# Optimization experiments

Hardware: AMD Instinct MI355X
Metric: run time of the kernel (lower is better)

## Reference

```python
import jax, jax.numpy as jnp
import numpy as np

N = 20000
E = 320000
IN_DIM = 16
H = 128
HEADS = 4
NEG_SLOPE = 0.2  # GATv2Conv default
EPS_LN = 1e-5


def setup_inputs() -> dict:
    key = jax.random.key(0)
    ks = jax.random.split(key, 16)
    f32 = jnp.float32
    def rn(k, shape, scale):
        return jax.random.normal(k, shape, dtype=f32) * scale
    s_in = 1.0 / np.sqrt(IN_DIM)
    s_h = 1.0 / np.sqrt(H)
    s_4h = 1.0 / np.sqrt(4 * H)
    s_2h = 1.0 / np.sqrt(2 * H)
    inp = {}
    inp["x"] = jax.random.normal(ks[0], (N, IN_DIM), dtype=f32)
    inp["edge_index"] = jax.random.randint(ks[1], (2, E), 0, N)
    inp["edge_attr"] = jax.random.normal(ks[2], (E, 2), dtype=f32)
    inp["emb_w"] = rn(ks[3], (IN_DIM, H), s_in)
    inp["emb_b"] = jnp.zeros((H,), f32)
    # 3 GATv2 layers stacked on leading axis
    inp["lin_l"] = rn(ks[4], (3, H, HEADS * H), s_h)
    inp["lin_r"] = rn(ks[5], (3, H, HEADS * H), s_h)
    inp["lin_edge"] = rn(ks[6], (3, 2, HEADS * H), 1.0 / np.sqrt(2.0))
    inp["att"] = rn(ks[7], (3, HEADS, H), s_h)
    inp["conv_bias01"] = jnp.zeros((2, HEADS * H), f32)  # concat=True layers
    inp["conv_bias2"] = jnp.zeros((H,), f32)             # concat=False layer
    inp["proj_w"] = rn(ks[8], (2, HEADS * H, H), s_4h)
    inp["proj_b"] = jnp.zeros((2, H), f32)
    inp["n1_g"] = jnp.ones((3, H), f32)
    inp["n1_b"] = jnp.zeros((3, H), f32)
    inp["n2_g"] = jnp.ones((3, H), f32)
    inp["n2_b"] = jnp.zeros((3, H), f32)
    inp["ffn_w1"] = rn(ks[9], (3, H, 2 * H), s_h)
    inp["ffn_b1"] = jnp.zeros((3, 2 * H), f32)
    inp["ffn_w2"] = rn(ks[10], (3, 2 * H, H), s_2h)
    inp["ffn_b2"] = jnp.zeros((3, H), f32)
    return inp


def layer_norm(x, g, b):
    mu = jnp.mean(x, axis=-1, keepdims=True)
    var = jnp.mean((x - mu) ** 2, axis=-1, keepdims=True)
    return (x - mu) * jax.lax.rsqrt(var + EPS_LN) * g + b


def gatv2(h, src, dst, eattr, Wl, Wr, We, att, bias, concat, n):
    # h: [n, H]; per-edge gather -> GATv2 attention -> segment softmax -> scatter-add
    xl = (h @ Wl).reshape(n, HEADS, H)   # source transform
    xr = (h @ Wr).reshape(n, HEADS, H)   # target transform
    ee = (eattr @ We).reshape(-1, HEADS, H)
    e = jax.nn.leaky_relu(xl[src] + xr[dst] + ee, NEG_SLOPE)  # [E', HEADS, H]
    score = jnp.einsum('ehc,hc->eh', e, att)                  # [E', HEADS]
    smax = jax.ops.segment_max(score, dst, num_segments=n)
    p = jnp.exp(score - smax[dst])
    denom = jax.ops.segment_sum(p, dst, num_segments=n)
    alpha = p / (denom[dst] + 1e-16)
    out = jax.ops.segment_sum(xl[src] * alpha[..., None], dst, num_segments=n)
    if concat:
        return out.reshape(n, HEADS * H) + bias
    return jnp.mean(out, axis=1) + bias


def reference(x, edge_index, edge_attr, emb_w, emb_b, lin_l, lin_r, lin_edge, att,
              conv_bias01, conv_bias2, proj_w, proj_b, n1_g, n1_b, n2_g, n2_b,
              ffn_w1, ffn_b1, ffn_w2, ffn_b2):
    n = x.shape[0]
    e = edge_attr.shape[0]
    # PyG add_self_loops with fill_value='mean': self-loop attr = mean of incoming edge attrs
    ones = jnp.ones((e,), x.dtype)
    deg = jax.ops.segment_sum(ones, edge_index[1], num_segments=n)
    loop_attr = jax.ops.segment_sum(edge_attr, edge_index[1], num_segments=n) / jnp.maximum(deg, 1.0)[:, None]
    ar = jnp.arange(n)
    src = jnp.concatenate([edge_index[0], ar])
    dst = jnp.concatenate([edge_index[1], ar])
    ea = jnp.concatenate([edge_attr, loop_attr], axis=0)

    h = x @ emb_w + emb_b
    for i in range(3):
        concat = i < 2
        bias = conv_bias01[i] if concat else conv_bias2
        h_in = h
        h = gatv2(h, src, dst, ea, lin_l[i], lin_r[i], lin_edge[i], att[i], bias, concat, n)
        if concat:
            h = h @ proj_w[i] + proj_b[i]
        h = layer_norm(h + h_in, n1_g[i], n1_b[i])
        h2 = h
        h = jax.nn.gelu(h @ ffn_w1[i] + ffn_b1[i], approximate=False) @ ffn_w2[i] + ffn_b2[i]
        h = layer_norm(h + h2, n2_g[i], n2_b[i])
    return h
```

## Files before the change

kernel.cpp:

```cpp
#include <hip/hip_runtime.h>
#include <math.h>

#define IN_DIM 16
#define HDIM   128
#define HEADS  4
#define HH     512
#define FFH    256
#define NEG_SLOPE 0.2f

typedef _Float16 half8 __attribute__((ext_vector_type(8)));
typedef _Float16 h8 __attribute__((ext_vector_type(8)));
typedef _Float16 h4 __attribute__((ext_vector_type(4)));
typedef _Float16 h2 __attribute__((ext_vector_type(2)));
typedef float f32x4 __attribute__((ext_vector_type(4)));

struct __align__(8) Edge { int src; _Float16 ea0, ea1; };

static __device__ inline float hsum8(h8 v) {
    h4 a = __builtin_shufflevector(v, v, 0, 1, 2, 3) +
           __builtin_shufflevector(v, v, 4, 5, 6, 7);
    h2 b = __builtin_shufflevector(a, a, 0, 1) +
           __builtin_shufflevector(a, a, 2, 3);
    return (float)b[0] + (float)b[1];
}

__global__ void xpad_kernel(const float* __restrict__ x, _Float16* __restrict__ xh, int n) {
    int idx = blockIdx.x * 256 + threadIdx.x;
    if (idx >= n * 64) return;
    int r = idx >> 6, k = idx & 63;
    xh[idx] = (k < IN_DIM) ? (_Float16)x[r * IN_DIM + k] : (_Float16)0.0f;
}

struct WDesc { const float* src; _Float16* dst; int Ksrc; int lgKd; int lgN; };
struct WDescs { WDesc d[15]; };
__global__ void wconv_kernel(WDescs ds) {
    WDesc w = ds.d[blockIdx.y];
    int Kd = 1 << w.lgKd;
    int total = 1 << (w.lgKd + w.lgN);
    for (int idx = blockIdx.x * 256 + threadIdx.x; idx < total; idx += gridDim.x * 256) {
        int n2 = idx >> w.lgKd, k = idx & (Kd - 1);
        w.dst[idx] = (k < w.Ksrc) ? (_Float16)w.src[(k << w.lgN) + n2] : (_Float16)0.0f;
    }
}

__global__ void deg_kernel(const int* __restrict__ ei, const float* __restrict__ eattr,
                           float* deg, float* asum, int E) {
    int e = blockIdx.x * blockDim.x + threadIdx.x;
    if (e >= E) return;
    int d = ei[E + e];
    atomicAdd(&deg[d], 1.0f);
    atomicAdd(&asum[2 * d], eattr[2 * e]);
    atomicAdd(&asum[2 * d + 1], eattr[2 * e + 1]);
}

__global__ void scan_kernel(const float* __restrict__ deg, int* row_ptr, int* cur, int n) {
    __shared__ int sums[1024];
    int tid = threadIdx.x;
    int per = (n + 1023) / 1024;
    int s0 = tid * per;
    int s1 = s0 + per; if (s1 > n) s1 = n;
    int s = 0;
    for (int i = s0; i < s1; i++) s += (int)deg[i] + 1;
    int mysum = s;
    sums[tid] = s;
    __syncthreads();
    for (int dd = 1; dd < 1024; dd <<= 1) {
        int t = (tid >= dd) ? sums[tid - dd] : 0;
        __syncthreads();
        sums[tid] += t;
        __syncthreads();
    }
    int run = sums[tid] - mysum;
    for (int i = s0; i < s1; i++) {
        row_ptr[i] = run; cur[i] = run;
        run += (int)deg[i] + 1;
    }
    if (tid == 1023) row_ptr[n] = sums[1023];
}

__global__ void scatter_kernel(const int* __restrict__ ei, const float* __restrict__ eattr,
                               const float* __restrict__ deg, const float* __restrict__ asum,
                               int* cur, Edge* csr, int E, int n) {
    int i = blockIdx.x * blockDim.x + threadIdx.x;
    if (i >= E + n) return;
    Edge ed;
    int pos;
    if (i < E) {
        int d = ei[E + i];
        pos = atomicAdd(&cur[d], 1);
        ed.src = ei[i];
        ed.ea0 = (_Float16)eattr[2 * i];
        ed.ea1 = (_Float16)eattr[2 * i + 1];
    } else {
        int nd = i - E;
        float dv = fmaxf(deg[nd], 1.0f);
        pos = atomicAdd(&cur[nd], 1);
        ed.src = nd;
        ed.ea0 = (_Float16)(asum[2 * nd] / dv);
        ed.ea1 = (_Float16)(asum[2 * nd + 1] / dv);
    }
    csr[pos] = ed;
}

template <int ACT, int OUTMODE, int BM>
__global__ __launch_bounds__(256) void gemm_mfma(const _Float16* __restrict__ A, int lda,
                                                 const _Float16* __restrict__ BT,
                                                 const float* __restrict__ bias,
                                                 float* __restrict__ C32,
                                                 _Float16* __restrict__ C16,
                                                 int M, int N, int K) {
    const int BK = 64, PAD = 8, NI = BM / 32;
    __shared__ _Float16 As[BM][BK + PAD];
    __shared__ _Float16 Bs[128][BK + PAD];
    int tid = threadIdx.x;
    int wave = tid >> 6, lane = tid & 63;
    int quad = lane >> 4, l16 = lane & 15;
    int wrow = (wave >> 1) * (16 * NI);
    int wcol = (wave & 1) * 64;
    int mBase = blockIdx.y * BM;
    int n0 = blockIdx.x * 128;

    f32x4 acc[NI][4] = {};

    for (int k0 = 0; k0 < K; k0 += BK) {
#pragma unroll
        for (int t = 0; t < BM / 32; t++) {
            int idx = tid + t * 256;
            int r = idx >> 3, kb = (idx & 7) * 8;
            half8 hv = {};
            int grow = mBase + r;
            if (grow < M) hv = *(const half8*)(A + (size_t)grow * lda + k0 + kb);
            *(half8*)&As[r][kb] = hv;
        }
#pragma unroll
        for (int t = 0; t < 4; t++) {
            int idx = tid + t * 256;
            int r = idx >> 3, kb = (idx & 7) * 8;
            *(half8*)&Bs[r][kb] = *(const half8*)(BT + (size_t)(n0 + r) * K + k0 + kb);
        }
        __syncthreads();
#pragma unroll
        for (int kc = 0; kc < 2; kc++) {
            half8 a[NI], b[4];
#pragma unroll
            for (int i = 0; i < NI; i++)
                a[i] = *(const half8*)&As[wrow + i * 16 + l16][kc * 32 + quad * 8];
#pragma unroll
            for (int j = 0; j < 4; j++)
                b[j] = *(const half8*)&Bs[wcol + j * 16 + l16][kc * 32 + quad * 8];
#pragma unroll
            for (int i = 0; i < NI; i++)
#pragma unroll
                for (int j = 0; j < 4; j++)
                    acc[i][j] = __builtin_amdgcn_mfma_f32_16x16x32_f16(a[i], b[j], acc[i][j], 0, 0, 0);
        }
        __syncthreads();
    }

#pragma unroll
    for (int i = 0; i < NI; i++) {
#pragma unroll
        for (int r = 0; r < 4; r++) {
            int row = mBase + wrow + i * 16 + quad * 4 + r;
            if (row >= M) continue;
#pragma unroll
            for (int j = 0; j < 4; j++) {
                int col = n0 + wcol + j * 16 + l16;
                float v = acc[i][j][r] + (bias ? bias[col] : 0.0f);
                if (ACT == 1) v = 0.5f * v * (1.0f + erff(v * 0.70710678118654752f));
                if (OUTMODE == 0 || OUTMODE == 2)
                    C32[(size_t)row * N + col] = v;
                if (OUTMODE == 1 || OUTMODE == 2)
                    C16[(size_t)row * N + col] = (_Float16)v;
            }
        }
    }
}

__global__ __launch_bounds__(256) void gemm_ln(const _Float16* __restrict__ A, int lda,
                                               const _Float16* __restrict__ BT,
                                               const float* __restrict__ bias,
                                               const float* __restrict__ R,
                                               const float* __restrict__ g,
                                               const float* __restrict__ b,
                                               float* __restrict__ C32,
                                               _Float16* __restrict__ C16,
                                               int M, int K) {
    const int BK = 64, PAD = 8;
    __shared__ _Float16 As[64][BK + PAD];
    __shared__ _Float16 Bs[128][BK + PAD];
    int tid = threadIdx.x;
    int wave = tid >> 6, lane = tid & 63;
    int quad = lane >> 4, l16 = lane & 15;
    int mBase = blockIdx.x * 64;

    f32x4 acc[8] = {};

    for (int k0 = 0; k0 < K; k0 += BK) {
#pragma unroll
        for (int t = 0; t < 2; t++) {
            int idx = tid + t * 256;
            int r = idx >> 3, kb = (idx & 7) * 8;
            half8 hv = {};
            int grow = mBase + r;
            if (grow < M) hv = *(const half8*)(A + (size_t)grow * lda + k0 + kb);
            *(half8*)&As[r][kb] = hv;
        }
#pragma unroll
        for (int t = 0; t < 4; t++) {
            int idx = tid + t * 256;
            int r = idx >> 3, kb = (idx & 7) * 8;
            *(half8*)&Bs[r][kb] = *(const half8*)(BT + (size_t)r * K + k0 + kb);
        }
        __syncthreads();
#pragma unroll
        for (int kc = 0; kc < 2; kc++) {
            half8 a = *(const half8*)&As[wave * 16 + l16][kc * 32 + quad * 8];
#pragma unroll
            for (int j = 0; j < 8; j++) {
                half8 bb = *(const half8*)&Bs[j * 16 + l16][kc * 32 + quad * 8];
                acc[j] = __builtin_amdgcn_mfma_f32_16x16x32_f16(a, bb, acc[j], 0, 0, 0);
            }
        }
        __syncthreads();
    }

    float gj[8], bj[8], biasj[8];
#pragma unroll
    for (int j = 0; j < 8; j++) {
        int col = j * 16 + l16;
        biasj[j] = bias[col];
        gj[j] = g[col];
        bj[j] = b[col];
    }
    int row0 = mBase + wave * 16 + quad * 4;
    float sum[4] = {}, sq[4] = {};
#pragma unroll
    for (int r = 0; r < 4; r++) {
        int row = row0 + r;
        bool ok = row < M;
        size_t base = (size_t)row * HDIM;
#pragma unroll
        for (int j = 0; j < 8; j++) {
            float v = acc[j][r] + biasj[j] + (ok ? R[base + j * 16 + l16] : 0.0f);
            acc[j][r] = v;
            sum[r] += v;
            sq[r] += v * v;
        }
    }
#pragma unroll
    for (int r = 0; r < 4; r++) {
#pragma unroll
        for (int off = 1; off < 16; off <<= 1) {
            sum[r] += __shfl_xor(sum[r], off);
            sq[r] += __shfl_xor(sq[r], off);
        }
    }
#pragma unroll
    for (int r = 0; r < 4; r++) {
        int row = row0 + r;
        if (row >= M) continue;
        size_t base = (size_t)row * HDIM;
        float mu = sum[r] * (1.0f / HDIM);
        float var = sq[r] * (1.0f / HDIM) - mu * mu;
        float invstd = rsqrtf(var + 1e-5f);
#pragma unroll
        for (int j = 0; j < 8; j++) {
            float o = (acc[j][r] - mu) * invstd * gj[j] + bj[j];
            C32[base + j * 16 + l16] = o;
            if (C16) C16[base + j * 16 + l16] = (_Float16)o;
        }
    }
}

__global__ __launch_bounds__(256) void gat_edge_kernel(
    const _Float16* __restrict__ XLR,
    const int* __restrict__ row_ptr, const Edge* __restrict__ csr,
    const float* __restrict__ We,
    const float* __restrict__ attW,
    const float* __restrict__ cbias,
    _Float16* __restrict__ OUT16, float* __restrict__ OUT32, int n, int concat) {
    int tid = threadIdx.x;
    int wave = tid >> 6, lane = tid & 63;
    int node = blockIdx.x * 4 + wave;
    if (node >= n) return;
    int c0 = lane * 8;

    h8 xr8 = *(const h8*)(XLR + (size_t)node * 1024 + 512 + c0);
    h8 w08, w18, att8;
#pragma unroll
    for (int k = 0; k < 8; k++) {
        w08[k] = (_Float16)We[c0 + k];
        w18[k] = (_Float16)We[HH + c0 + k];
        att8[k] = (_Float16)attW[c0 + k];
    }
    const _Float16 slope = (_Float16)NEG_SLOPE;

    h8 acc2 = (h8)(_Float16)0.0f;
    float m = -INFINITY, l = 0.0f;
    int beg = row_ptr[node], end = row_ptr[node + 1];
    int j = beg;
    for (; j + 1 < end; j += 2) {
        Edge e0 = csr[j], e1 = csr[j + 1];
        h8 x0 = *(const h8*)(XLR + (size_t)e0.src * 1024 + c0);
        h8 x1 = *(const h8*)(XLR + (size_t)e1.src * 1024 + c0);
        h8 v0 = x0 + (xr8 + w08 * e0.ea0 + w18 * e0.ea1);
        h8 v1 = x1 + (xr8 + w08 * e1.ea0 + w18 * e1.ea1);
        v0 = __builtin_elementwise_max(v0, v0 * slope);
        v1 = __builtin_elementwise_max(v1, v1 * slope);
        float p0 = hsum8(v0 * att8);
        float p1 = hsum8(v1 * att8);
        p0 += __shfl_xor(p0, 1); p1 += __shfl_xor(p1, 1);
        p0 += __shfl_xor(p0, 2); p1 += __shfl_xor(p1, 2);
        p0 += __shfl_xor(p0, 4); p1 += __shfl_xor(p1, 4);
        p0 += __shfl_xor(p0, 8); p1 += __shfl_xor(p1, 8);
        float mnew = fmaxf(m, fmaxf(p0, p1));
        float sc = __expf(m - mnew);
        float e0f = __expf(p0 - mnew);
        float e1f = __expf(p1 - mnew);
        l = l * sc + e0f + e1f;
        acc2 = acc2 * (_Float16)sc + x0 * (_Float16)e0f + x1 * (_Float16)e1f;
        m = mnew;
    }
    if (j < end) {
        Edge e0 = csr[j];
        h8 x0 = *(const h8*)(XLR + (size_t)e0.src * 1024 + c0);
        h8 v0 = x0 + (xr8 + w08 * e0.ea0 + w18 * e0.ea1);
        v0 = __builtin_elementwise_max(v0, v0 * slope);
        float p0 = hsum8(v0 * att8);
        p0 += __shfl_xor(p0, 1);
        p0 += __shfl_xor(p0, 2);
        p0 += __shfl_xor(p0, 4);
        p0 += __shfl_xor(p0, 8);
        float mnew = fmaxf(m, p0);
        float sc = __expf(m - mnew);
        float e0f = __expf(p0 - mnew);
        l = l * sc + e0f;
        acc2 = acc2 * (_Float16)sc + x0 * (_Float16)e0f;
        m = mnew;
    }
    float invf = 1.0f / (l + 1e-16f);
    if (concat) {
        h8 o = acc2 * (_Float16)invf;
#pragma unroll
        for (int k = 0; k < 8; k++) o[k] = o[k] + (_Float16)cbias[c0 + k];
        *(h8*)(OUT16 + (size_t)node * 1024 + c0) = o;
    } else {
        float o8[8];
#pragma unroll
        for (int k = 0; k < 8; k++) {
            float a = (float)acc2[k] * invf;
            a += __shfl_xor(a, 16);
            a += __shfl_xor(a, 32);
            o8[k] = a;
        }
        if (lane < 16) {
#pragma unroll
            for (int k = 0; k < 8; k++)
                OUT32[(size_t)node * HDIM + c0 + k] = o8[k] * 0.25f + cbias[c0 + k];
        }
    }
}

__global__ __launch_bounds__(256) void ln_res_kernel(const float* X, const float* R,
                                                     const float* __restrict__ g,
                                                     const float* __restrict__ b,
                                                     float* OUT32, _Float16* OUT16, int n) {
    int wave = threadIdx.x >> 6, lane = threadIdx.x & 63;
    int row = blockIdx.x * 4 + wave;
    if (row >= n) return;
    int c = lane * 2;
    size_t base = (size_t)row * HDIM;
    float x0 = X[base + c] + R[base + c];
    float x1 = X[base + c + 1] + R[base + c + 1];
    float s = x0 + x1;
#pragma unroll
    for (int off = 1; off < 64; off <<= 1) s += __shfl_xor(s, off);
    float mu = s * (1.0f / HDIM);
    float d0 = x0 - mu, d1 = x1 - mu;
    float vs = d0 * d0 + d1 * d1;
#pragma unroll
    for (int off = 1; off < 64; off <<= 1) vs += __shfl_xor(vs, off);
    float invstd = rsqrtf(vs * (1.0f / HDIM) + 1e-5f);
    float o0 = d0 * invstd * g[c] + b[c];
    float o1 = d1 * invstd * g[c + 1] + b[c + 1];
    OUT32[base + c] = o0;
    OUT32[base + c + 1] = o1;
    if (OUT16) {
        OUT16[base + c] = (_Float16)o0;
        OUT16[base + c + 1] = (_Float16)o1;
    }
}

extern "C" void kernel_launch(void* const* d_in, const int* in_sizes, int n_in,
                              void* d_out, int out_size, void* d_ws, size_t ws_size,
                              hipStream_t stream) {
    const float* x        = (const float*)d_in[0];
    const int*   ei       = (const int*)d_in[1];
    const float* eattr    = (const float*)d_in[2];
    const float* emb_w    = (const float*)d_in[3];
    const float* emb_b    = (const float*)d_in[4];
    const float* lin_l    = (const float*)d_in[5];
    const float* lin_r    = (const float*)d_in[6];
    const float* lin_edge = (const float*)d_in[7];
    const float* attw     = (const float*)d_in[8];
    const float* cb01     = (const float*)d_in[9];
    const float* cb2      = (const float*)d_in[10];
    const float* proj_w   = (const float*)d_in[11];
    const float* proj_b   = (const float*)d_in[12];
    const float* n1g      = (const float*)d_in[13];
    const float* n1b      = (const float*)d_in[14];
    const float* n2g      = (const float*)d_in[15];
    const float* n2b      = (const float*)d_in[16];
    const float* fw1      = (const float*)d_in[17];
    const float* fb1      = (const float*)d_in[18];
    const float* fw2      = (const float*)d_in[19];
    const float* fb2      = (const float*)d_in[20];
    float* out = (float*)d_out;

    const int n = in_sizes[0] / IN_DIM;
    const int E = in_sizes[2] / 2;
    const int EP = E + n;

    size_t off = 0;
    auto alloc = [&](size_t bytes) {
        void* p = (char*)d_ws + off;
        off += (bytes + 255) & ~(size_t)255;
        return p;
    };
    float* deg     = (float*)alloc((size_t)n * 4);
    float* asum    = (float*)alloc((size_t)2 * n * 4);
    int*   row_ptr = (int*)alloc((size_t)(n + 1) * 4);
    int*   cur     = (int*)alloc((size_t)n * 4);
    Edge*  csr     = (Edge*)alloc((size_t)EP * 8);
    float* H0      = (float*)alloc((size_t)n * HDIM * 4);
    float* H1      = (float*)alloc((size_t)n * HDIM * 4);
    _Float16* H0h  = (_Float16*)alloc((size_t)n * HDIM * 2);
    _Float16* H1h  = (_Float16*)alloc((size_t)n * HDIM * 2);
    _Float16* MID  = (_Float16*)alloc((size_t)n * FFH * 2);
    _Float16* XLR  = (_Float16*)alloc((size_t)n * 1024 * 2);
    _Float16* xh   = (_Float16*)alloc((size_t)n * 64 * 2);
    _Float16* wt_emb  = (_Float16*)alloc((size_t)HDIM * 64 * 2);
    _Float16* wt_llr  = (_Float16*)alloc((size_t)3 * 1024 * HDIM * 2);
    _Float16* wt_proj = (_Float16*)alloc((size_t)2 * HDIM * HH * 2);
    _Float16* wt_f1   = (_Float16*)alloc((size_t)3 * FFH * HDIM * 2);
    _Float16* wt_f2   = (_Float16*)alloc((size_t)3 * HDIM * FFH * 2);
    (void)ws_size;

    xpad_kernel<<<(n * 64 + 255) / 256, 256, 0, stream>>>(x, xh, n);
    WDescs ds;
    int di = 0;
    ds.d[di++] = {emb_w, wt_emb, IN_DIM, 6, 7};
    for (int i = 0; i < 3; i++) {
        ds.d[di++] = {lin_l + (size_t)i * HDIM * HH, wt_llr + (size_t)i * 1024 * HDIM, HDIM, 7, 9};
        ds.d[di++] = {lin_r + (size_t)i * HDIM * HH, wt_llr + (size_t)i * 1024 * HDIM + (size_t)512 * HDIM, HDIM, 7, 9};
    }
    for (int i = 0; i < 2; i++)
        ds.d[di++] = {proj_w + (size_t)i * HH * HDIM, wt_proj + (size_t)i * HDIM * HH, HH, 9, 7};
    for (int i = 0; i < 3; i++)
        ds.d[di++] = {fw1 + (size_t)i * HDIM * FFH, wt_f1 + (size_t)i * FFH * HDIM, HDIM, 7, 8};
    for (int i = 0; i < 3; i++)
        ds.d[di++] = {fw2 + (size_t)i * FFH * HDIM, wt_f2 + (size_t)i * HDIM * FFH, FFH, 8, 7};
    wconv_kernel<<<dim3(32, 15), 256, 0, stream>>>(ds);

    (void)hipMemsetAsync(deg, 0, (size_t)n * 4, stream);
    (void)hipMemsetAsync(asum, 0, (size_t)2 * n * 4, stream);
    deg_kernel<<<(E + 255) / 256, 256, 0, stream>>>(ei, eattr, deg, asum, E);
    scan_kernel<<<1, 1024, 0, stream>>>(deg, row_ptr, cur, n);
    scatter_kernel<<<(EP + 255) / 256, 256, 0, stream>>>(ei, eattr, deg, asum, cur, csr, E, n);

    gemm_mfma<0, 2, 128><<<dim3(1, (n + 127) / 128), 256, 0, stream>>>(
        xh, 64, wt_emb, emb_b, H0, H0h, n, HDIM, 64);

    for (int i = 0; i < 3; i++) {
        int concat = (i < 2);
        gemm_mfma<0, 1, 128><<<dim3(8, (n + 127) / 128), 256, 0, stream>>>(
            H0h, HDIM, wt_llr + (size_t)i * 1024 * HDIM, nullptr, nullptr, XLR, n, 1024, HDIM);
        gat_edge_kernel<<<(n + 3) / 4, 256, 0, stream>>>(
            XLR, row_ptr, csr,
            lin_edge + (size_t)i * 2 * HH, attw + (size_t)i * HH,
            concat ? (cb01 + (size_t)i * HH) : cb2,
            XLR + 512, H1, n, concat);
        if (concat) {
            gemm_ln<<<(n + 63) / 64, 256, 0, stream>>>(
                XLR + 512, 1024, wt_proj + (size_t)i * HDIM * HH,
                proj_b + (size_t)i * HDIM, H0,
                n1g + (size_t)i * HDIM, n1b + (size_t)i * HDIM,
                H1, H1h, n, HH);
        } else {
            ln_res_kernel<<<(n + 3) / 4, 256, 0, stream>>>(
                H1, H0, n1g + (size_t)i * HDIM, n1b + (size_t)i * HDIM, H1, H1h, n);
        }
        gemm_mfma<1, 1, 128><<<dim3(2, (n + 127) / 128), 256, 0, stream>>>(
            H1h, HDIM, wt_f1 + (size_t)i * FFH * HDIM, fb1 + (size_t)i * FFH,
            nullptr, MID, n, FFH, HDIM);
        float* lnout = (i == 2) ? out : H0;
        _Float16* lnout16 = (i == 2) ? nullptr : H0h;
        gemm_ln<<<(n + 63) / 64, 256, 0, stream>>>(
            MID, FFH, wt_f2 + (size_t)i * HDIM * FFH, fb2 + (size_t)i * HDIM, H1,
            n2g + (size_t)i * HDIM, n2b + (size_t)i * HDIM,
            lnout, lnout16, n, FFH);
    }
}
```

Before: 659.6 us.

## Fuse FFN GEMMs with GELU in shared memory and fold final LayerNorm into GAT kernel

Adds an ffn_fused kernel that computes the first FFN GEMM with bias and GELU, keeps the 64x256 intermediate in shared memory, then runs the second GEMM with bias, residual and LayerNorm. This removes the global MID buffer round trip and one launch per layer. The non-concat GAT layer now applies its residual LayerNorm directly in the edge kernel, so the separate ln_res_kernel launch goes away. The costs are reloading weight tiles per 64-row block, more shared memory per block (lower occupancy), and a serialized GEMM chain inside one block.

```diff
diff --git a/kernel.cpp b/kernel.cpp
--- a/kernel.cpp
+++ b/kernel.cpp
@@ -102,7 +102,7 @@
     csr[pos] = ed;
 }
 
-template <int ACT, int OUTMODE, int BM>
+template <int OUTMODE, int BM>
 __global__ __launch_bounds__(256) void gemm_mfma(const _Float16* __restrict__ A, int lda,
                                                  const _Float16* __restrict__ BT,
                                                  const float* __restrict__ bias,
@@ -167,7 +167,6 @@
             for (int j = 0; j < 4; j++) {
                 int col = n0 + wcol + j * 16 + l16;
                 float v = acc[i][j][r] + (bias ? bias[col] : 0.0f);
-                if (ACT == 1) v = 0.5f * v * (1.0f + erff(v * 0.70710678118654752f));
                 if (OUTMODE == 0 || OUTMODE == 2)
                     C32[(size_t)row * N + col] = v;
                 if (OUTMODE == 1 || OUTMODE == 2)
@@ -273,13 +272,148 @@
     }
 }
 
+__global__ __launch_bounds__(256) void ffn_fused(const _Float16* __restrict__ A,
+                                                 const _Float16* __restrict__ W1T,
+                                                 const float* __restrict__ b1,
+                                                 const _Float16* __restrict__ W2T,
+                                                 const float* __restrict__ b2,
+                                                 const float* __restrict__ R,
+                                                 const float* __restrict__ g,
+                                                 const float* __restrict__ b,
+                                                 float* __restrict__ C32,
+                                                 _Float16* __restrict__ C16,
+                                                 int M) {
+    __shared__ _Float16 Ws[128][128 + 8];
+    __shared__ _Float16 Mid[64][256 + 8];
+    int tid = threadIdx.x;
+    int wave = tid >> 6, lane = tid & 63;
+    int quad = lane >> 4, l16 = lane & 15;
+    int mBase = blockIdx.x * 64;
+
+    half8 afrag[4];
+    {
+        int row = mBase + wave * 16 + l16;
+#pragma unroll
+        for (int kc = 0; kc < 4; kc++) {
+            if (row < M)
+                afrag[kc] = *(const half8*)(A + (size_t)row * HDIM + kc * 32 + quad * 8);
+            else
+                afrag[kc] = (half8)(_Float16)0.0f;
+        }
+    }
+
+#pragma unroll
+    for (int h = 0; h < 2; h++) {
+        if (h) __syncthreads();
+#pragma unroll
+        for (int t = 0; t < 8; t++) {
+            int idx = tid + t * 256;
+            int r = idx >> 4, kb = (idx & 15) * 8;
+            *(half8*)&Ws[r][kb] = *(const half8*)(W1T + (size_t)(h * 128 + r) * HDIM + kb);
+        }
+        __syncthreads();
+        f32x4 acc[8] = {};
+#pragma unroll
+        for (int kc = 0; kc < 4; kc++) {
+#pragma unroll
+            for (int j = 0; j < 8; j++) {
+                half8 bb = *(const half8*)&Ws[j * 16 + l16][kc * 32 + quad * 8];
+                acc[j] = __builtin_amdgcn_mfma_f32_16x16x32_f16(afrag[kc], bb, acc[j], 0, 0, 0);
+            }
+        }
+#pragma unroll
+        for (int j = 0; j < 8; j++) {
+            float bj1 = b1[h * 128 + j * 16 + l16];
+#pragma unroll
+            for (int r = 0; r < 4; r++) {
+                float v = acc[j][r] + bj1;
+                v = 0.5f * v * (1.0f + erff(v * 0.70710678118654752f));
+                Mid[wave * 16 + quad * 4 + r][h * 128 + j * 16 + l16] = (_Float16)v;
+            }
+        }
+    }
+    __syncthreads();
+
+    f32x4 acc2[8] = {};
+#pragma unroll
+    for (int kc2 = 0; kc2 < 2; kc2++) {
+        if (kc2) __syncthreads();
+#pragma unroll
+        for (int t = 0; t < 8; t++) {
+            int idx = tid + t * 256;
+            int r = idx >> 4, kb = (idx & 15) * 8;
+            *(half8*)&Ws[r][kb] = *(const half8*)(W2T + (size_t)r * FFH + kc2 * 128 + kb);
+        }
+        __syncthreads();
+#pragma unroll
+        for (int kc = 0; kc < 4; kc++) {
+            half8 am = *(const half8*)&Mid[wave * 16 + l16][kc2 * 128 + kc * 32 + quad * 8];
+#pragma unroll
+            for (int j = 0; j < 8; j++) {
+                half8 bb = *(const half8*)&Ws[j * 16 + l16][kc * 32 + quad * 8];
+                acc2[j] = __builtin_amdgcn_mfma_f32_16x16x32_f16(am, bb, acc2[j], 0, 0, 0);
+            }
+        }
+    }
+
+    float gj[8], bj[8], b2j[8];
+#pragma unroll
+    for (int j = 0; j < 8; j++) {
+        int col = j * 16 + l16;
+        b2j[j] = b2[col];
+        gj[j] = g[col];
+        bj[j] = b[col];
+    }
+    int row0 = mBase + wave * 16 + quad * 4;
+    float sum[4] = {}, sq[4] = {};
+#pragma unroll
+    for (int r = 0; r < 4; r++) {
+        int row = row0 + r;
+        bool ok = row < M;
+        size_t base = (size_t)row * HDIM;
+#pragma unroll
+        for (int j = 0; j < 8; j++) {
+            float v = acc2[j][r] + b2j[j] + (ok ? R[base + j * 16 + l16] : 0.0f);
+            acc2[j][r] = v;
+            sum[r] += v;
+            sq[r] += v * v;
+        }
+    }
+#pragma unroll
+    for (int r = 0; r < 4; r++) {
+#pragma unroll
+        for (int off = 1; off < 16; off <<= 1) {
+            sum[r] += __shfl_xor(sum[r], off);
+            sq[r] += __shfl_xor(sq[r], off);
+        }
+    }
+#pragma unroll
+    for (int r = 0; r < 4; r++) {
+        int row = row0 + r;
+        if (row >= M) continue;
+        size_t base = (size_t)row * HDIM;
+        float mu = sum[r] * (1.0f / HDIM);
+        float var = sq[r] * (1.0f / HDIM) - mu * mu;
+        float invstd = rsqrtf(var + 1e-5f);
+#pragma unroll
+        for (int j = 0; j < 8; j++) {
+            float o = (acc2[j][r] - mu) * invstd * gj[j] + bj[j];
+            C32[base + j * 16 + l16] = o;
+            if (C16) C16[base + j * 16 + l16] = (_Float16)o;
+        }
+    }
+}
+
 __global__ __launch_bounds__(256) void gat_edge_kernel(
     const _Float16* __restrict__ XLR,
     const int* __restrict__ row_ptr, const Edge* __restrict__ csr,
     const float* __restrict__ We,
     const float* __restrict__ attW,
     const float* __restrict__ cbias,
-    _Float16* __restrict__ OUT16, float* __restrict__ OUT32, int n, int concat) {
+    _Float16* __restrict__ OUT16, float* __restrict__ OUT32,
+    const float* __restrict__ R, const float* __restrict__ lng,
+    const float* __restrict__ lnb, _Float16* __restrict__ OUT16h,
+    int n, int concat) {
     int tid = threadIdx.x;
     int wave = tid >> 6, lane = tid & 63;
     int node = blockIdx.x * 4 + wave;
@@ -354,41 +488,33 @@
             a += __shfl_xor(a, 32);
             o8[k] = a;
         }
+        float v8[8];
+        float sum = 0.0f, sq = 0.0f;
         if (lane < 16) {
 #pragma unroll
-            for (int k = 0; k < 8; k++)
-                OUT32[(size_t)node * HDIM + c0 + k] = o8[k] * 0.25f + cbias[c0 + k];
-        }
-    }
-}
-
-__global__ __launch_bounds__(256) void ln_res_kernel(const float* X, const float* R,
-                                                     const float* __restrict__ g,
-                                                     const float* __restrict__ b,
-                                                     float* OUT32, _Float16* OUT16, int n) {
-    int wave = threadIdx.x >> 6, lane = threadIdx.x & 63;
-    int row = blockIdx.x * 4 + wave;
-    if (row >= n) return;
-    int c = lane * 2;
-    size_t base = (size_t)row * HDIM;
-    float x0 = X[base + c] + R[base + c];
-    float x1 = X[base + c + 1] + R[base + c + 1];
-    float s = x0 + x1;
-#pragma unroll
-    for (int off = 1; off < 64; off <<= 1) s += __shfl_xor(s, off);
-    float mu = s * (1.0f / HDIM);
-    float d0 = x0 - mu, d1 = x1 - mu;
-    float vs = d0 * d0 + d1 * d1;
-#pragma unroll
-    for (int off = 1; off < 64; off <<= 1) vs += __shfl_xor(vs, off);
-    float invstd = rsqrtf(vs * (1.0f / HDIM) + 1e-5f);
-    float o0 = d0 * invstd * g[c] + b[c];
-    float o1 = d1 * invstd * g[c + 1] + b[c + 1];
-    OUT32[base + c] = o0;
-    OUT32[base + c + 1] = o1;
-    if (OUT16) {
-        OUT16[base + c] = (_Float16)o0;
-        OUT16[base + c + 1] = (_Float16)o1;
+            for (int k = 0; k < 8; k++) {
+                float v = o8[k] * 0.25f + cbias[c0 + k] + R[(size_t)node * HDIM + c0 + k];
+                v8[k] = v;
+                sum += v;
+                sq += v * v;
+            }
+        }
+#pragma unroll
+        for (int off = 1; off < 16; off <<= 1) {
+            sum += __shfl_xor(sum, off);
+            sq += __shfl_xor(sq, off);
+        }
+        if (lane < 16) {
+            float mu = sum * (1.0f / HDIM);
+            float var = sq * (1.0f / HDIM) - mu * mu;
+            float invstd = rsqrtf(var + 1e-5f);
+#pragma unroll
+            for (int k = 0; k < 8; k++) {
+                float o = (v8[k] - mu) * invstd * lng[c0 + k] + lnb[c0 + k];
+                OUT32[(size_t)node * HDIM + c0 + k] = o;
+                OUT16h[(size_t)node * HDIM + c0 + k] = (_Float16)o;
+            }
+        }
     }
 }
 
@@ -437,7 +563,6 @@
     float* H1      = (float*)alloc((size_t)n * HDIM * 4);
     _Float16* H0h  = (_Float16*)alloc((size_t)n * HDIM * 2);
     _Float16* H1h  = (_Float16*)alloc((size_t)n * HDIM * 2);
-    _Float16* MID  = (_Float16*)alloc((size_t)n * FFH * 2);
     _Float16* XLR  = (_Float16*)alloc((size_t)n * 1024 * 2);
     _Float16* xh   = (_Float16*)alloc((size_t)n * 64 * 2);
     _Float16* wt_emb  = (_Float16*)alloc((size_t)HDIM * 64 * 2);
@@ -469,36 +594,33 @@
     scan_kernel<<<1, 1024, 0, stream>>>(deg, row_ptr, cur, n);
     scatter_kernel<<<(EP + 255) / 256, 256, 0, stream>>>(ei, eattr, deg, asum, cur, csr, E, n);
 
-    gemm_mfma<0, 2, 128><<<dim3(1, (n + 127) / 128), 256, 0, stream>>>(
+    gemm_mfma<2, 128><<<dim3(1, (n + 127) / 128), 256, 0, stream>>>(
         xh, 64, wt_emb, emb_b, H0, H0h, n, HDIM, 64);
 
     for (int i = 0; i < 3; i++) {
         int concat = (i < 2);
-        gemm_mfma<0, 1, 128><<<dim3(8, (n + 127) / 128), 256, 0, stream>>>(
+        gemm_mfma<1, 128><<<dim3(8, (n + 127) / 128), 256, 0, stream>>>(
             H0h, HDIM, wt_llr + (size_t)i * 1024 * HDIM, nullptr, nullptr, XLR, n, 1024, HDIM);
         gat_edge_kernel<<<(n + 3) / 4, 256, 0, stream>>>(
             XLR, row_ptr, csr,
             lin_edge + (size_t)i * 2 * HH, attw + (size_t)i * HH,
             concat ? (cb01 + (size_t)i * HH) : cb2,
-            XLR + 512, H1, n, concat);
+            XLR + 512, H1,
+            H0, n1g + (size_t)i * HDIM, n1b + (size_t)i * HDIM, H1h,
+            n, concat);
         if (concat) {
             gemm_ln<<<(n + 63) / 64, 256, 0, stream>>>(
                 XLR + 512, 1024, wt_proj + (size_t)i * HDIM * HH,
                 proj_b + (size_t)i * HDIM, H0,
                 n1g + (size_t)i * HDIM, n1b + (size_t)i * HDIM,
                 H1, H1h, n, HH);
-        } else {
-            ln_res_kernel<<<(n + 3) / 4, 256, 0, stream>>>(
-                H1, H0, n1g + (size_t)i * HDIM, n1b + (size_t)i * HDIM, H1, H1h, n);
-        }
-        gemm_mfma<1, 1, 128><<<dim3(2, (n + 127) / 128), 256, 0, stream>>>(
-            H1h, HDIM, wt_f1 + (size_t)i * FFH * HDIM, fb1 + (size_t)i * FFH,
-            nullptr, MID, n, FFH, HDIM);
+        }
         float* lnout = (i == 2) ? out : H0;
         _Float16* lnout16 = (i == 2) ? nullptr : H0h;
-        gemm_ln<<<(n + 63) / 64, 256, 0, stream>>>(
-            MID, FFH, wt_f2 + (size_t)i * HDIM * FFH, fb2 + (size_t)i * HDIM, H1,
+        ffn_fused<<<(n + 63) / 64, 256, 0, stream>>>(
+            H1h, wt_f1 + (size_t)i * FFH * HDIM, fb1 + (size_t)i * FFH,
+            wt_f2 + (size_t)i * HDIM * FFH, fb2 + (size_t)i * HDIM, H1,
             n2g + (size_t)i * HDIM, n2b + (size_t)i * HDIM,
-            lnout, lnout16, n, FFH);
-    }
-}
+            lnout, lnout16, n);
+    }
+}
```

After: 600.2 us. -9.0%, faster.
